# Kernel tuning notes

Hardware: AMD Instinct MI355X
Metric: run time of the kernel (lower is better)

The kernel has to match this reference:

```python
import jax, jax.numpy as jnp
import numpy as np
import math

B, L, V, D, H, DQ, DV, DI, NL, BOARD = 2048, 10, 1974, 512, 8, 64, 64, 2048, 6, 70
SCALE = 0.02

def _ln(x, g, b):
    m = x.mean(-1, keepdims=True)
    v = ((x - m) ** 2).mean(-1, keepdims=True)
    return (x - m) * jax.lax.rsqrt(v + 1e-5) * g + b

def _mha(x, kv, ln_g, ln_b, wq, bq, wkv, bkv, wo, bo, key_mask, causal, self_attn):
    # residual + pre-LN multi-head attention, as in the torch module (dropout in eval mode = identity)
    res = x
    xn = _ln(x, ln_g, ln_b)
    kvn = _ln(kv, ln_g, ln_b) if self_attn else kv  # torch code layer-norms KV only for self-attention
    b, lq, _ = x.shape
    lk = kv.shape[1]
    q = (xn @ wq + bq).reshape(b, lq, H, DQ)
    kvp = kvn @ wkv + bkv
    k = kvp[..., : H * DQ].reshape(b, lk, H, DQ)
    v = kvp[..., H * DQ :].reshape(b, lk, H, DV)
    s = jnp.einsum('bqhd,bkhd->bhqk', q, k) * (1.0 / math.sqrt(DQ))  # (B,H,Lq,Lk)
    if key_mask is not None:
        s = jnp.where(key_mask[:, None, None, :], s, -jnp.inf)
    if causal:
        s = jnp.where(jnp.tril(jnp.ones((lq, lk), bool)), s, -jnp.inf)
    a = jax.nn.softmax(s, axis=-1)
    o = jnp.einsum('bhqk,bkhd->bqhd', a, v).reshape(b, lq, H * DV)
    return o @ wo + bo + res

def _ffn(x, ln_g, ln_b, w1, b1, w2, b2):
    h = jax.nn.relu(_ln(x, ln_g, ln_b) @ w1 + b1)
    return h @ w2 + b2 + x

def _forward(moves, lengths, boards, emb, pos, sa_ln_g, sa_ln_b, sa_wq, sa_bq, sa_wkv, sa_bkv, sa_wo, sa_bo, ca_ln_g, ca_ln_b, ca_wq, ca_bq, ca_wkv, ca_bkv, ca_wo, ca_bo, ff_ln_g, ff_ln_b, ff_w1, ff_b1, ff_w2, ff_b2, fin_g, fin_b, fc_w, fc_b):
    x = emb[moves] * math.sqrt(D) + pos[None, :, :]  # (B,L,D)
    key_mask = jnp.arange(L)[None, :] < lengths[:, None]  # (B,L) valid move positions
    for i in range(NL):
        x = _mha(x, x, sa_ln_g[i], sa_ln_b[i], sa_wq[i], sa_bq[i], sa_wkv[i], sa_bkv[i], sa_wo[i], sa_bo[i], key_mask, True, True)
        x = _mha(x, boards, ca_ln_g[i], ca_ln_b[i], ca_wq[i], ca_bq[i], ca_wkv[i], ca_bkv[i], ca_wo[i], ca_bo[i], None, False, False)
        x = _ffn(x, ff_ln_g[i], ff_ln_b[i], ff_w1[i], ff_b1[i], ff_w2[i], ff_b2[i])
    x = _ln(x, fin_g, fin_b)
    return x @ fc_w + fc_b  # (B,L,V) logits

def setup_inputs():
    key = jax.random.key(0)
    ks = iter(jax.random.split(key, 40))
    n = lambda shape: jax.random.normal(next(ks), shape, dtype=jnp.float32) * SCALE
    return {
        'moves': jax.random.randint(next(ks), (B, L), 0, V),
        'lengths': jax.random.randint(next(ks), (B,), 1, L + 1),
        'boards': jax.random.normal(next(ks), (B, BOARD, D), dtype=jnp.float32),
        'emb': n((V, D)),
        'pos': n((L, D)),
        'sa_ln_g': jnp.ones((NL, D)), 'sa_ln_b': jnp.zeros((NL, D)),
        'sa_wq': n((NL, D, H * DQ)), 'sa_bq': jnp.zeros((NL, H * DQ)),
        'sa_wkv': n((NL, D, H * (DQ + DV))), 'sa_bkv': jnp.zeros((NL, H * (DQ + DV))),
        'sa_wo': n((NL, H * DV, D)), 'sa_bo': jnp.zeros((NL, D)),
        'ca_ln_g': jnp.ones((NL, D)), 'ca_ln_b': jnp.zeros((NL, D)),
        'ca_wq': n((NL, D, H * DQ)), 'ca_bq': jnp.zeros((NL, H * DQ)),
        'ca_wkv': n((NL, D, H * (DQ + DV))), 'ca_bkv': jnp.zeros((NL, H * (DQ + DV))),
        'ca_wo': n((NL, H * DV, D)), 'ca_bo': jnp.zeros((NL, D)),
        'ff_ln_g': jnp.ones((NL, D)), 'ff_ln_b': jnp.zeros((NL, D)),
        'ff_w1': n((NL, D, DI)), 'ff_b1': jnp.zeros((NL, DI)),
        'ff_w2': n((NL, DI, D)), 'ff_b2': jnp.zeros((NL, D)),
        'fin_g': jnp.ones((D,)), 'fin_b': jnp.zeros((D,)),
        'fc_w': n((D, V)), 'fc_b': jnp.zeros((V,)),
    }

def reference(moves, lengths, boards, emb, pos, sa_ln_g, sa_ln_b, sa_wq, sa_bq, sa_wkv, sa_bkv, sa_wo, sa_bo, ca_ln_g, ca_ln_b, ca_wq, ca_bq, ca_wkv, ca_bkv, ca_wo, ca_bo, ff_ln_g, ff_ln_b, ff_w1, ff_b1, ff_w2, ff_b2, fin_g, fin_b, fc_w, fc_b):
    return _forward(moves, lengths, boards, emb, pos, sa_ln_g, sa_ln_b, sa_wq, sa_bq, sa_wkv, sa_bkv, sa_wo, sa_bo, ca_ln_g, ca_ln_b, ca_wq, ca_bq, ca_wkv, ca_bkv, ca_wo, ca_bo, ff_ln_g, ff_ln_b, ff_w1, ff_b1, ff_w2, ff_b2, fin_g, fin_b, fc_w, fc_b)
```

## Files before the change

kernel.cpp:

```cpp
#include <hip/hip_runtime.h>
#include <math.h>

#define B_     2048
#define L_     10
#define D_     512
#define H_     8
#define V_     1974
#define DI_    2048
#define NL_    6
#define BOARD_ 70
#define ROWS_  (B_ * L_)
#define SQRT_D 22.627416997969522f

typedef __attribute__((ext_vector_type(8))) short s16x8;
typedef __attribute__((ext_vector_type(4))) float f32x4;

__device__ __forceinline__ void split2(float x, short &hi, short &lo)
{
    unsigned u = __float_as_uint(x);
    hi = (short)(u >> 16);
    float hf = __uint_as_float(u & 0xffff0000u);
    lo = (short)(__float_as_uint(x - hf) >> 16);
}

__global__ __launch_bounds__(256)
void embed_k(const int* __restrict__ moves, const float* __restrict__ emb,
             const float* __restrict__ pos, float* __restrict__ X)
{
    int idx = blockIdx.x * 256 + threadIdx.x;
    if (idx >= ROWS_ * D_) return;
    int d  = idx & 511;
    int bl = idx >> 9;
    int l  = bl % L_;
    int mv = moves[bl];
    X[idx] = emb[mv * D_ + d] * SQRT_D + pos[l * D_ + d];
}

__global__ __launch_bounds__(256)
void ln_k(const float* __restrict__ X, const float* __restrict__ g,
          const float* __restrict__ bta, float* __restrict__ Y, int rows)
{
    int wave = threadIdx.x >> 6;
    int lane = threadIdx.x & 63;
    int row  = blockIdx.x * 4 + wave;
    if (row >= rows) return;
    const float* x = X + (size_t)row * D_;
    float4 t0 = *(const float4*)&x[lane * 8];
    float4 t1 = *(const float4*)&x[lane * 8 + 4];
    float v[8] = { t0.x, t0.y, t0.z, t0.w, t1.x, t1.y, t1.z, t1.w };
    float s1 = 0.f, s2 = 0.f;
    #pragma unroll
    for (int q = 0; q < 8; q++) { s1 += v[q]; s2 += v[q] * v[q]; }
    #pragma unroll
    for (int off = 32; off; off >>= 1) {
        s1 += __shfl_xor(s1, off);
        s2 += __shfl_xor(s2, off);
    }
    float m   = s1 * (1.f / D_);
    float var = s2 * (1.f / D_) - m * m;
    float r   = 1.0f / sqrtf(var + 1e-5f);
    float* y = Y + (size_t)row * D_;
    #pragma unroll
    for (int q = 0; q < 8; q++) {
        int d = lane * 8 + q;
        y[d] = (v[q] - m) * r * g[d] + bta[d];
    }
}

__global__ __launch_bounds__(256)
void tsplit_k(const float* __restrict__ W, short* __restrict__ Thi,
              short* __restrict__ Tlo, int K, int N)
{
    __shared__ float t[32][33];
    int n0 = blockIdx.x * 32, k0 = blockIdx.y * 32;
    int c = threadIdx.x & 31, r = threadIdx.x >> 5;
    #pragma unroll
    for (int i = 0; i < 4; i++) {
        int kk = k0 + r + i * 8, nn = n0 + c;
        t[r + i * 8][c] = (nn < N) ? W[(size_t)kk * N + nn] : 0.f;
    }
    __syncthreads();
    #pragma unroll
    for (int i = 0; i < 4; i++) {
        int nn = n0 + r + i * 8;
        int kk = k0 + c;
        if (nn < N) {
            short hi, lo; split2(t[c][r + i * 8], hi, lo);
            Thi[(size_t)nn * K + kk] = hi;
            Tlo[(size_t)nn * K + kk] = lo;
        }
    }
}

template<bool BIAS, bool RELU, bool RESID>
__global__ __launch_bounds__(256)
void mgemm_k(const float* __restrict__ A,
             const short* __restrict__ BThi, const short* __restrict__ BTlo,
             const float* __restrict__ bias, const float* __restrict__ resid,
             float* __restrict__ C, int M, int N, int K)
{
    __shared__ short Ah[4][128][8], Al[4][128][8];
    __shared__ short Bh[4][128][8], Bl[4][128][8];

    const int tid = threadIdx.x;
    const int m0 = blockIdx.y * 128, n0 = blockIdx.x * 128;

    const int ar   = tid >> 2;
    const int akg  = tid & 3;
    const int bc   = tid >> 1;
    const int bkg0 = tid & 1;

    const int lane = tid & 63;
    const int wv   = tid >> 6;
    const int wm   = (wv >> 1) * 64, wn = (wv & 1) * 64;
    const int rsel = lane & 15, kg = lane >> 4;

    f32x4 acc[4][4];
    #pragma unroll
    for (int i = 0; i < 4; i++)
        #pragma unroll
        for (int j = 0; j < 4; j++)
            #pragma unroll
            for (int q = 0; q < 4; q++) acc[i][j][q] = 0.f;

    const s16x8 *pAh[4], *pAl[4], *pBh[4], *pBl[4];
    #pragma unroll
    for (int x = 0; x < 4; x++) {
        pAh[x] = (const s16x8*)&Ah[kg][wm + x * 16 + rsel][0];
        pAl[x] = (const s16x8*)&Al[kg][wm + x * 16 + rsel][0];
        pBh[x] = (const s16x8*)&Bh[kg][wn + x * 16 + rsel][0];
        pBl[x] = (const s16x8*)&Bl[kg][wn + x * 16 + rsel][0];
    }

    f32x4 pa[2][2];
    s16x8 pbh[2], pbl[2];

    auto loadA = [&](int k0) {
        #pragma unroll
        for (int p = 0; p < 2; p++) {
            const float* ap = A + (size_t)(m0 + ar + p * 64) * K + k0 + akg * 8;
            pa[p][0] = *(const f32x4*)ap;
            pa[p][1] = *(const f32x4*)(ap + 4);
        }
    };
    auto loadB = [&](int k0) {
        #pragma unroll
        for (int p = 0; p < 2; p++) {
            int col = n0 + bc, kgp = bkg0 + p * 2;
            if (col < N) {
                size_t off = (size_t)col * K + k0 + kgp * 8;
                pbh[p] = *(const s16x8*)(BThi + off);
                pbl[p] = *(const s16x8*)(BTlo + off);
            } else {
                #pragma unroll
                for (int q = 0; q < 8; q++) { pbh[p][q] = 0; pbl[p][q] = 0; }
            }
        }
    };
    auto storeLDS = [&]() {
        #pragma unroll
        for (int p = 0; p < 2; p++) {
            s16x8 h, l;
            #pragma unroll
            for (int q = 0; q < 8; q++) {
                float x = (q < 4) ? pa[p][0][q] : pa[p][1][q - 4];
                short hh, ll; split2(x, hh, ll);
                h[q] = hh; l[q] = ll;
            }
            *(s16x8*)&Ah[akg][ar + p * 64][0] = h;
            *(s16x8*)&Al[akg][ar + p * 64][0] = l;
            *(s16x8*)&Bh[bkg0 + p * 2][bc][0] = pbh[p];
            *(s16x8*)&Bl[bkg0 + p * 2][bc][0] = pbl[p];
        }
    };

    loadA(0); loadB(0);
    const int nk = K >> 5;
    for (int t = 0; t < nk; t++) {
        __syncthreads();
        storeLDS();
        __syncthreads();
        if (t + 1 < nk) { loadA((t + 1) << 5); loadB((t + 1) << 5); }

        s16x8 a_hi[4], b_hi[4], tmp[4];
        #pragma unroll
        for (int x = 0; x < 4; x++) a_hi[x] = *pAh[x];
        #pragma unroll
        for (int x = 0; x < 4; x++) b_hi[x] = *pBh[x];
        #pragma unroll
        for (int mt = 0; mt < 4; mt++)
            #pragma unroll
            for (int nt = 0; nt < 4; nt++)
                acc[mt][nt] = __builtin_amdgcn_mfma_f32_16x16x32_bf16(
                    a_hi[mt], b_hi[nt], acc[mt][nt], 0, 0, 0);
        #pragma unroll
        for (int x = 0; x < 4; x++) tmp[x] = *pBl[x];
        #pragma unroll
        for (int mt = 0; mt < 4; mt++)
            #pragma unroll
            for (int nt = 0; nt < 4; nt++)
                acc[mt][nt] = __builtin_amdgcn_mfma_f32_16x16x32_bf16(
                    a_hi[mt], tmp[nt], acc[mt][nt], 0, 0, 0);
        #pragma unroll
        for (int x = 0; x < 4; x++) tmp[x] = *pAl[x];
        #pragma unroll
        for (int mt = 0; mt < 4; mt++)
            #pragma unroll
            for (int nt = 0; nt < 4; nt++)
                acc[mt][nt] = __builtin_amdgcn_mfma_f32_16x16x32_bf16(
                    tmp[mt], b_hi[nt], acc[mt][nt], 0, 0, 0);
    }

    #pragma unroll
    for (int mt = 0; mt < 4; mt++) {
        #pragma unroll
        for (int q = 0; q < 4; q++) {
            int m = m0 + wm + mt * 16 + kg * 4 + q;
            #pragma unroll
            for (int nt = 0; nt < 4; nt++) {
                int n = n0 + wn + nt * 16 + rsel;
                if (n < N) {
                    float v = acc[mt][nt][q];
                    if (BIAS)  v += bias[n];
                    if (RELU)  v = fmaxf(v, 0.f);
                    if (RESID) v += resid[(size_t)m * N + n];
                    C[(size_t)m * N + n] = v;
                }
            }
        }
    }
}

template<bool BIAS, bool RELU, bool RESID>
__global__ __launch_bounds__(256)
void gemm_k(const float* __restrict__ A, const float* __restrict__ Bw,
            const float* __restrict__ bias, const float* __restrict__ resid,
            float* __restrict__ C, int M, int N, int K)
{
    __shared__ float As[8][128];
    __shared__ float Bs[8][128];
    const int tid = threadIdx.x;
    const int tx = tid & 15, ty = tid >> 4;
    const int m0 = blockIdx.y * 128, n0 = blockIdx.x * 128;
    float acc[8][8] = {};
    const int arow = tid >> 1;
    const int akk  = (tid & 1) * 4;
    const int brow = tid >> 5;
    const int bcol = (tid & 31) * 4;
    const int am   = m0 + arow;

    for (int k0 = 0; k0 < K; k0 += 8) {
        float a4[4];
        if (am < M) {
            const float* ap = A + (size_t)am * K + k0 + akk;
            float4 t = *(const float4*)ap;
            a4[0] = t.x; a4[1] = t.y; a4[2] = t.z; a4[3] = t.w;
        } else { a4[0] = a4[1] = a4[2] = a4[3] = 0.f; }
        #pragma unroll
        for (int q = 0; q < 4; q++) As[akk + q][arow] = a4[q];
        {
            const int nb = n0 + bcol;
            const float* bp = Bw + (size_t)(k0 + brow) * N + nb;
            float b4[4];
            if (nb + 3 < N) {
                float2 u0 = *(const float2*)bp;
                float2 u1 = *(const float2*)(bp + 2);
                b4[0] = u0.x; b4[1] = u0.y; b4[2] = u1.x; b4[3] = u1.y;
            } else {
                #pragma unroll
                for (int q = 0; q < 4; q++) b4[q] = (nb + q < N) ? bp[q] : 0.f;
            }
            #pragma unroll
            for (int q = 0; q < 4; q++) Bs[brow][bcol + q] = b4[q];
        }
        __syncthreads();
        #pragma unroll
        for (int kk = 0; kk < 8; kk++) {
            float4 a0 = *(const float4*)&As[kk][ty * 8];
            float4 a1 = *(const float4*)&As[kk][ty * 8 + 4];
            float4 b0 = *(const float4*)&Bs[kk][tx * 8];
            float4 b1 = *(const float4*)&Bs[kk][tx * 8 + 4];
            float av[8] = {a0.x,a0.y,a0.z,a0.w,a1.x,a1.y,a1.z,a1.w};
            float bv[8] = {b0.x,b0.y,b0.z,b0.w,b1.x,b1.y,b1.z,b1.w};
            #pragma unroll
            for (int i = 0; i < 8; i++)
                #pragma unroll
                for (int j = 0; j < 8; j++)
                    acc[i][j] += av[i] * bv[j];
        }
        __syncthreads();
    }
    #pragma unroll
    for (int i = 0; i < 8; i++) {
        int m = m0 + ty * 8 + i;
        if (m >= M) continue;
        #pragma unroll
        for (int j = 0; j < 8; j++) {
            int n = n0 + tx * 8 + j;
            if (n >= N) continue;
            float v = acc[i][j];
            if (BIAS)  v += bias[n];
            if (RELU)  v = fmaxf(v, 0.f);
            if (RESID) v += resid[(size_t)m * N + n];
            C[(size_t)m * N + n] = v;
        }
    }
}

__global__ __launch_bounds__(256)
void self_attn_k(const float* __restrict__ Qb, const float* __restrict__ KVP,
                 const int* __restrict__ lengths, float* __restrict__ O, int b0)
{
    __shared__ float qs[L_ * D_];
    __shared__ float ks[L_ * D_];
    __shared__ float vs[L_ * D_];
    __shared__ float sc[H_ * L_ * L_];
    int bl  = blockIdx.x;
    int b   = b0 + bl;
    int tid = threadIdx.x;
    int len = lengths[b];

    for (int p = tid; p < L_ * D_; p += 256) {
        int row = p >> 9, col = p & 511;
        qs[p] = Qb[((size_t)(b * L_ + row)) * D_ + col];
        ks[p] = KVP[((size_t)(bl * L_ + row)) * 1024 + col];
        vs[p] = KVP[((size_t)(bl * L_ + row)) * 1024 + 512 + col];
    }
    __syncthreads();

    for (int p = tid; p < H_ * L_ * L_; p += 256) {
        int h = p / (L_ * L_), r = p % (L_ * L_), i = r / L_, j = r % L_;
        float s = -1e30f;
        if (j <= i && j < len) {
            const float* qq = &qs[i * D_ + h * 64];
            const float* kk = &ks[j * D_ + h * 64];
            float d = 0.f;
            #pragma unroll
            for (int d0 = 0; d0 < 64; d0++) d += qq[d0] * kk[d0];
            s = d * 0.125f;
        }
        sc[p] = s;
    }
    __syncthreads();

    if (tid < H_ * L_) {
        int base = tid * L_;
        float mx = -1e30f;
        for (int j = 0; j < L_; j++) mx = fmaxf(mx, sc[base + j]);
        float sum = 0.f;
        for (int j = 0; j < L_; j++) { float e = expf(sc[base + j] - mx); sc[base + j] = e; sum += e; }
        float inv = 1.f / sum;
        for (int j = 0; j < L_; j++) sc[base + j] *= inv;
    }
    __syncthreads();

    for (int p = tid; p < L_ * D_; p += 256) {
        int i = p >> 9, col = p & 511, h = col >> 6;
        float o = 0.f;
        #pragma unroll
        for (int j = 0; j < L_; j++) o += sc[(h * L_ + i) * L_ + j] * vs[j * D_ + col];
        O[((size_t)(b * L_ + i)) * D_ + col] = o;
    }
}

__global__ __launch_bounds__(256)
void cross_attn_k(const float* __restrict__ Qb, const float* __restrict__ KVP,
                  float* __restrict__ O, int b0)
{
    __shared__ float qs[L_ * 64];
    __shared__ float ks[BOARD_ * 64];
    __shared__ float vs[BOARD_ * 64];
    __shared__ float sc[L_ * BOARD_];
    int blk = blockIdx.x;
    int bl  = blk >> 3;
    int h   = blk & 7;
    int b   = b0 + bl;
    int tid = threadIdx.x;

    for (int p = tid; p < L_ * 64; p += 256) {
        int i = p >> 6, d = p & 63;
        qs[p] = Qb[((size_t)(b * L_ + i)) * D_ + h * 64 + d];
    }
    for (int p = tid; p < BOARD_ * 64; p += 256) {
        int j = p >> 6, d = p & 63;
        size_t kr = (size_t)(bl * BOARD_ + j);
        ks[p] = KVP[kr * 1024 + h * 64 + d];
        vs[p] = KVP[kr * 1024 + 512 + h * 64 + d];
    }
    __syncthreads();

    for (int p = tid; p < L_ * BOARD_; p += 256) {
        int i = p / BOARD_, j = p % BOARD_;
        float d = 0.f;
        #pragma unroll
        for (int d0 = 0; d0 < 64; d0++) d += qs[i * 64 + d0] * ks[j * 64 + d0];
        sc[p] = d * 0.125f;
    }
    __syncthreads();

    if (tid < L_) {
        float mx = -1e30f;
        for (int j = 0; j < BOARD_; j++) mx = fmaxf(mx, sc[tid * BOARD_ + j]);
        float sum = 0.f;
        for (int j = 0; j < BOARD_; j++) {
            float e = expf(sc[tid * BOARD_ + j] - mx);
            sc[tid * BOARD_ + j] = e; sum += e;
        }
        float inv = 1.f / sum;
        for (int j = 0; j < BOARD_; j++) sc[tid * BOARD_ + j] *= inv;
    }
    __syncthreads();

    for (int p = tid; p < L_ * 64; p += 256) {
        int i = p >> 6, d = p & 63;
        float o = 0.f;
        for (int j = 0; j < BOARD_; j++) o += sc[i * BOARD_ + j] * vs[j * 64 + d];
        O[((size_t)(b * L_ + i)) * D_ + h * 64 + d] = o;
    }
}

extern "C" void kernel_launch(void* const* d_in, const int* in_sizes, int n_in,
                              void* d_out, int out_size, void* d_ws, size_t ws_size,
                              hipStream_t stream)
{
    (void)in_sizes; (void)n_in; (void)out_size;
    const int*   moves   = (const int*)d_in[0];
    const int*   lengths = (const int*)d_in[1];
    const float* boards  = (const float*)d_in[2];
    const float* emb     = (const float*)d_in[3];
    const float* pos     = (const float*)d_in[4];
    const float* sa_ln_g = (const float*)d_in[5];
    const float* sa_ln_b = (const float*)d_in[6];
    const float* sa_wq   = (const float*)d_in[7];
    const float* sa_bq   = (const float*)d_in[8];
    const float* sa_wkv  = (const float*)d_in[9];
    const float* sa_bkv  = (const float*)d_in[10];
    const float* sa_wo   = (const float*)d_in[11];
    const float* sa_bo   = (const float*)d_in[12];
    const float* ca_ln_g = (const float*)d_in[13];
    const float* ca_ln_b = (const float*)d_in[14];
    const float* ca_wq   = (const float*)d_in[15];
    const float* ca_bq   = (const float*)d_in[16];
    const float* ca_wkv  = (const float*)d_in[17];
    const float* ca_bkv  = (const float*)d_in[18];
    const float* ca_wo   = (const float*)d_in[19];
    const float* ca_bo   = (const float*)d_in[20];
    const float* ff_ln_g = (const float*)d_in[21];
    const float* ff_ln_b = (const float*)d_in[22];
    const float* ff_w1   = (const float*)d_in[23];
    const float* ff_b1   = (const float*)d_in[24];
    const float* ff_w2   = (const float*)d_in[25];
    const float* ff_b2   = (const float*)d_in[26];
    const float* fin_g   = (const float*)d_in[27];
    const float* fin_b   = (const float*)d_in[28];
    const float* fc_w    = (const float*)d_in[29];
    const float* fc_b    = (const float*)d_in[30];

    float* X  = (float*)d_out;
    float* Q  = X + (size_t)ROWS_ * D_;
    float* U  = Q + (size_t)ROWS_ * D_;
    const size_t WSLAB = (size_t)2048 * 512;
    short* WThi = (short*)(U + (size_t)17920 * 1024);
    short* WTlo = WThi + WSLAB;
    short* QThi = (short*)Q;
    short* QTlo = QThi + WSLAB;
    float* XN = (float*)d_ws;
    short* FThi = (short*)(XN + (size_t)ROWS_ * D_);
    short* FTlo = FThi + WSLAB;
    const bool ws_wt = ws_size >= (size_t)ROWS_ * D_ * 4 + 2 * WSLAB * sizeof(short);

    const int lnGrid = ROWS_ / 4;
    #define TGRID(N, K) dim3(((N) + 31) / 32, (K) / 32)

    embed_k<<<(ROWS_ * D_ + 255) / 256, 256, 0, stream>>>(moves, emb, pos, X);

    for (int i = 0; i < NL_; i++) {
        ln_k<<<lnGrid, 256, 0, stream>>>(X, sa_ln_g + i * D_, sa_ln_b + i * D_, XN, ROWS_);
        tsplit_k<<<TGRID(512, 512), 256, 0, stream>>>(sa_wq + (size_t)i * D_ * 512, WThi, WTlo, 512, 512);
        mgemm_k<true, false, false><<<dim3(4, 160), 256, 0, stream>>>(
            XN, WThi, WTlo, sa_bq + i * 512, nullptr, Q, ROWS_, 512, 512);
        tsplit_k<<<TGRID(1024, 512), 256, 0, stream>>>(sa_wkv + (size_t)i * D_ * 1024, WThi, WTlo, 512, 1024);
        for (int c = 0; c < 2; c++) {
            const int RB = 1024, RR = RB * L_;
            mgemm_k<true, false, false><<<dim3(8, RR / 128), 256, 0, stream>>>(
                XN + (size_t)c * RR * D_, WThi, WTlo, sa_bkv + i * 1024, nullptr,
                U, RR, 1024, 512);
            self_attn_k<<<RB, 256, 0, stream>>>(Q, U, lengths, XN, c * RB);
        }
        tsplit_k<<<TGRID(512, 512), 256, 0, stream>>>(sa_wo + (size_t)i * 512 * D_, WThi, WTlo, 512, 512);
        mgemm_k<true, false, true><<<dim3(4, 160), 256, 0, stream>>>(
            XN, WThi, WTlo, sa_bo + i * D_, X, X, ROWS_, 512, 512);

        ln_k<<<lnGrid, 256, 0, stream>>>(X, ca_ln_g + i * D_, ca_ln_b + i * D_, XN, ROWS_);
        tsplit_k<<<TGRID(512, 512), 256, 0, stream>>>(ca_wq + (size_t)i * D_ * 512, WThi, WTlo, 512, 512);
        mgemm_k<true, false, false><<<dim3(4, 160), 256, 0, stream>>>(
            XN, WThi, WTlo, ca_bq + i * 512, nullptr, Q, ROWS_, 512, 512);
        tsplit_k<<<TGRID(1024, 512), 256, 0, stream>>>(ca_wkv + (size_t)i * D_ * 1024, WThi, WTlo, 512, 1024);
        for (int c = 0; c < B_ / 256; c++) {
            const int CHB = 256, KR = CHB * BOARD_;
            mgemm_k<true, false, false><<<dim3(8, KR / 128), 256, 0, stream>>>(
                boards + (size_t)c * KR * D_, WThi, WTlo, ca_bkv + i * 1024, nullptr,
                U, KR, 1024, 512);
            cross_attn_k<<<CHB * H_, 256, 0, stream>>>(Q, U, XN, c * CHB);
        }
        tsplit_k<<<TGRID(512, 512), 256, 0, stream>>>(ca_wo + (size_t)i * 512 * D_, WThi, WTlo, 512, 512);
        mgemm_k<true, false, true><<<dim3(4, 160), 256, 0, stream>>>(
            XN, WThi, WTlo, ca_bo + i * D_, X, X, ROWS_, 512, 512);

        ln_k<<<lnGrid, 256, 0, stream>>>(X, ff_ln_g + i * D_, ff_ln_b + i * D_, XN, ROWS_);
        tsplit_k<<<TGRID(2048, 512), 256, 0, stream>>>(ff_w1 + (size_t)i * D_ * DI_, QThi, QTlo, 512, 2048);
        tsplit_k<<<TGRID(512, 2048), 256, 0, stream>>>(ff_w2 + (size_t)i * DI_ * D_, WThi, WTlo, 2048, 512);
        for (int rc = 0; rc < 4; rc++) {
            const int RC = ROWS_ / 4;
            mgemm_k<true, true, false><<<dim3(16, RC / 128), 256, 0, stream>>>(
                XN + (size_t)rc * RC * D_, QThi, QTlo, ff_b1 + i * DI_, nullptr,
                U, RC, DI_, 512);
            mgemm_k<true, false, true><<<dim3(4, RC / 128), 256, 0, stream>>>(
                U, WThi, WTlo, ff_b2 + i * D_,
                X + (size_t)rc * RC * D_, X + (size_t)rc * RC * D_, RC, 512, DI_);
        }
    }

    ln_k<<<lnGrid, 256, 0, stream>>>(X, fin_g, fin_b, XN, ROWS_);
    if (ws_wt) {
        tsplit_k<<<TGRID(V_, 512), 256, 0, stream>>>(fc_w, FThi, FTlo, 512, V_);
        mgemm_k<true, false, false><<<dim3((V_ + 127) / 128, 160), 256, 0, stream>>>(
            XN, FThi, FTlo, fc_b, nullptr, (float*)d_out, ROWS_, V_, 512);
    } else {
        gemm_k<true, false, false><<<dim3((V_ + 127) / 128, 160), 256, 0, stream>>>(
            XN, fc_w, fc_b, nullptr, (float*)d_out, ROWS_, V_, 512);
    }
}
```

Before: 15.59 ms.

## Rewrite split-bf16 GEMM with 32x32 MFMA, direct-to-LDS B loads, double buffering

Replaces the split-bf16 MFMA GEMM with a new kernel that uses 32x32x16 MFMA tiles, loads the pre-split weight operand straight into LDS with global_load_lds, and double-buffers the B tile so the next K-step load overlaps compute. It also XOR-swizzles the A tile in LDS to avoid bank conflicts, puts M on the x grid axis, and allows wider N tiles (256) with two blocks per CU. The bounds check in tsplit is removed and the FC split is padded to 2048 columns, so the workspace must hold the padded FC weights. The unguarded B loads rely on the padded N. In exchange the kernel has more register pressure and depends on the workspace padding being correct.

```diff
diff --git a/kernel.cpp b/kernel.cpp
--- a/kernel.cpp
+++ b/kernel.cpp
@@ -12,8 +12,9 @@
 #define ROWS_  (B_ * L_)
 #define SQRT_D 22.627416997969522f
 
-typedef __attribute__((ext_vector_type(8))) short s16x8;
-typedef __attribute__((ext_vector_type(4))) float f32x4;
+typedef __attribute__((ext_vector_type(8)))  short s16x8;
+typedef __attribute__((ext_vector_type(4)))  float f32x4;
+typedef __attribute__((ext_vector_type(16))) float f32x16;
 
 __device__ __forceinline__ void split2(float x, short &hi, short &lo)
 {
@@ -22,6 +23,15 @@
     float hf = __uint_as_float(u & 0xffff0000u);
     lo = (short)(__float_as_uint(x - hf) >> 16);
 }
+
+__device__ __forceinline__ void gload_lds16(const void* g, void* l)
+{
+    __builtin_amdgcn_global_load_lds(
+        (const __attribute__((address_space(1))) unsigned int*)g,
+        (__attribute__((address_space(3))) unsigned int*)l, 16, 0, 0);
+}
+
+__device__ __forceinline__ int gofs(int kg) { return ((kg & 1) << 2) | (kg & 2); }
 
 __global__ __launch_bounds__(256)
 void embed_k(const int* __restrict__ moves, const float* __restrict__ emb,
@@ -84,57 +94,43 @@
     for (int i = 0; i < 4; i++) {
         int nn = n0 + r + i * 8;
         int kk = k0 + c;
-        if (nn < N) {
-            short hi, lo; split2(t[c][r + i * 8], hi, lo);
-            Thi[(size_t)nn * K + kk] = hi;
-            Tlo[(size_t)nn * K + kk] = lo;
-        }
-    }
-}
-
-template<bool BIAS, bool RELU, bool RESID>
-__global__ __launch_bounds__(256)
-void mgemm_k(const float* __restrict__ A,
-             const short* __restrict__ BThi, const short* __restrict__ BTlo,
-             const float* __restrict__ bias, const float* __restrict__ resid,
-             float* __restrict__ C, int M, int N, int K)
-{
+        short hi, lo; split2(t[c][r + i * 8], hi, lo);
+        Thi[(size_t)nn * K + kk] = hi;
+        Tlo[(size_t)nn * K + kk] = lo;
+    }
+}
+
+template<int BN, bool BIAS, bool RELU, bool RESID>
+__global__ __launch_bounds__(256, 2)
+void mg2_k(const float* __restrict__ A,
+           const short* __restrict__ BThi, const short* __restrict__ BTlo,
+           const float* __restrict__ bias, const float* __restrict__ resid,
+           float* __restrict__ C, int M, int N, int K)
+{
+    constexpr int NF = BN / 64;
     __shared__ short Ah[4][128][8], Al[4][128][8];
-    __shared__ short Bh[4][128][8], Bl[4][128][8];
-
-    const int tid = threadIdx.x;
-    const int m0 = blockIdx.y * 128, n0 = blockIdx.x * 128;
-
-    const int ar   = tid >> 2;
-    const int akg  = tid & 3;
-    const int bc   = tid >> 1;
-    const int bkg0 = tid & 1;
-
+    __shared__ short Bh[2][4][BN][8], Bl[2][4][BN][8];
+
+    const int tid  = threadIdx.x;
     const int lane = tid & 63;
     const int wv   = tid >> 6;
-    const int wm   = (wv >> 1) * 64, wn = (wv & 1) * 64;
-    const int rsel = lane & 15, kg = lane >> 4;
-
-    f32x4 acc[4][4];
-    #pragma unroll
-    for (int i = 0; i < 4; i++)
-        #pragma unroll
-        for (int j = 0; j < 4; j++)
-            #pragma unroll
-            for (int q = 0; q < 4; q++) acc[i][j][q] = 0.f;
-
-    const s16x8 *pAh[4], *pAl[4], *pBh[4], *pBl[4];
-    #pragma unroll
-    for (int x = 0; x < 4; x++) {
-        pAh[x] = (const s16x8*)&Ah[kg][wm + x * 16 + rsel][0];
-        pAl[x] = (const s16x8*)&Al[kg][wm + x * 16 + rsel][0];
-        pBh[x] = (const s16x8*)&Bh[kg][wn + x * 16 + rsel][0];
-        pBl[x] = (const s16x8*)&Bl[kg][wn + x * 16 + rsel][0];
-    }
+    const int m0 = blockIdx.x * 128, n0 = blockIdx.y * BN;
+
+    const int ar  = tid >> 2;
+    const int akg = tid & 3;
+
+    const int wm  = (wv >> 1) * 64, wn = (wv & 1) * (BN / 2);
+    const int l31 = lane & 31, lhi = lane >> 5;
+
+    f32x16 acc[2][NF];
+    #pragma unroll
+    for (int mf = 0; mf < 2; mf++)
+        #pragma unroll
+        for (int nf = 0; nf < NF; nf++)
+            #pragma unroll
+            for (int r = 0; r < 16; r++) acc[mf][nf][r] = 0.f;
 
     f32x4 pa[2][2];
-    s16x8 pbh[2], pbl[2];
-
     auto loadA = [&](int k0) {
         #pragma unroll
         for (int p = 0; p < 2; p++) {
@@ -143,21 +139,8 @@
             pa[p][1] = *(const f32x4*)(ap + 4);
         }
     };
-    auto loadB = [&](int k0) {
-        #pragma unroll
-        for (int p = 0; p < 2; p++) {
-            int col = n0 + bc, kgp = bkg0 + p * 2;
-            if (col < N) {
-                size_t off = (size_t)col * K + k0 + kgp * 8;
-                pbh[p] = *(const s16x8*)(BThi + off);
-                pbl[p] = *(const s16x8*)(BTlo + off);
-            } else {
-                #pragma unroll
-                for (int q = 0; q < 8; q++) { pbh[p][q] = 0; pbl[p][q] = 0; }
-            }
-        }
-    };
-    auto storeLDS = [&]() {
+    auto storeA = [&]() {
+        const int g = gofs(akg);
         #pragma unroll
         for (int p = 0; p < 2; p++) {
             s16x8 h, l;
@@ -167,61 +150,84 @@
                 short hh, ll; split2(x, hh, ll);
                 h[q] = hh; l[q] = ll;
             }
-            *(s16x8*)&Ah[akg][ar + p * 64][0] = h;
-            *(s16x8*)&Al[akg][ar + p * 64][0] = l;
-            *(s16x8*)&Bh[bkg0 + p * 2][bc][0] = pbh[p];
-            *(s16x8*)&Bl[bkg0 + p * 2][bc][0] = pbl[p];
+            const int row = (ar + p * 64) ^ g;
+            *(s16x8*)&Ah[akg][row][0] = h;
+            *(s16x8*)&Al[akg][row][0] = l;
         }
     };
-
-    loadA(0); loadB(0);
+    auto issueB = [&](int k0, int bb) {
+        #pragma unroll
+        for (int cb = 0; cb < NF; cb++) {
+            const size_t go = (size_t)(n0 + cb * 64 + lane) * K + k0 + wv * 8;
+            gload_lds16(BThi + go, &Bh[bb][wv][cb * 64][0]);
+            gload_lds16(BTlo + go, &Bl[bb][wv][cb * 64][0]);
+        }
+    };
+    auto compute = [&](int bb) {
+        #pragma unroll
+        for (int ks = 0; ks < 2; ks++) {
+            const int kg = 2 * ks + lhi;
+            const int g  = gofs(kg);
+            s16x8 ah[2], bh[NF], bl[NF], al[2];
+            #pragma unroll
+            for (int mf = 0; mf < 2; mf++)
+                ah[mf] = *(const s16x8*)&Ah[kg][(wm + mf * 32 + l31) ^ g][0];
+            #pragma unroll
+            for (int nf = 0; nf < NF; nf++)
+                bh[nf] = *(const s16x8*)&Bh[bb][kg][wn + nf * 32 + l31][0];
+            #pragma unroll
+            for (int mf = 0; mf < 2; mf++)
+                #pragma unroll
+                for (int nf = 0; nf < NF; nf++)
+                    acc[mf][nf] = __builtin_amdgcn_mfma_f32_32x32x16_bf16(
+                        ah[mf], bh[nf], acc[mf][nf], 0, 0, 0);
+            #pragma unroll
+            for (int nf = 0; nf < NF; nf++)
+                bl[nf] = *(const s16x8*)&Bl[bb][kg][wn + nf * 32 + l31][0];
+            #pragma unroll
+            for (int mf = 0; mf < 2; mf++)
+                #pragma unroll
+                for (int nf = 0; nf < NF; nf++)
+                    acc[mf][nf] = __builtin_amdgcn_mfma_f32_32x32x16_bf16(
+                        ah[mf], bl[nf], acc[mf][nf], 0, 0, 0);
+            #pragma unroll
+            for (int mf = 0; mf < 2; mf++)
+                al[mf] = *(const s16x8*)&Al[kg][(wm + mf * 32 + l31) ^ g][0];
+            #pragma unroll
+            for (int mf = 0; mf < 2; mf++)
+                #pragma unroll
+                for (int nf = 0; nf < NF; nf++)
+                    acc[mf][nf] = __builtin_amdgcn_mfma_f32_32x32x16_bf16(
+                        al[mf], bh[nf], acc[mf][nf], 0, 0, 0);
+        }
+    };
+
+    issueB(0, 0);
+    loadA(0);
+    __syncthreads();
     const int nk = K >> 5;
     for (int t = 0; t < nk; t++) {
+        storeA();
         __syncthreads();
-        storeLDS();
+        if (t + 1 < nk) {
+            issueB((t + 1) << 5, (t + 1) & 1);
+            loadA((t + 1) << 5);
+        }
+        compute(t & 1);
         __syncthreads();
-        if (t + 1 < nk) { loadA((t + 1) << 5); loadB((t + 1) << 5); }
-
-        s16x8 a_hi[4], b_hi[4], tmp[4];
-        #pragma unroll
-        for (int x = 0; x < 4; x++) a_hi[x] = *pAh[x];
-        #pragma unroll
-        for (int x = 0; x < 4; x++) b_hi[x] = *pBh[x];
-        #pragma unroll
-        for (int mt = 0; mt < 4; mt++)
-            #pragma unroll
-            for (int nt = 0; nt < 4; nt++)
-                acc[mt][nt] = __builtin_amdgcn_mfma_f32_16x16x32_bf16(
-                    a_hi[mt], b_hi[nt], acc[mt][nt], 0, 0, 0);
-        #pragma unroll
-        for (int x = 0; x < 4; x++) tmp[x] = *pBl[x];
-        #pragma unroll
-        for (int mt = 0; mt < 4; mt++)
-            #pragma unroll
-            for (int nt = 0; nt < 4; nt++)
-                acc[mt][nt] = __builtin_amdgcn_mfma_f32_16x16x32_bf16(
-                    a_hi[mt], tmp[nt], acc[mt][nt], 0, 0, 0);
-        #pragma unroll
-        for (int x = 0; x < 4; x++) tmp[x] = *pAl[x];
-        #pragma unroll
-        for (int mt = 0; mt < 4; mt++)
-            #pragma unroll
-            for (int nt = 0; nt < 4; nt++)
-                acc[mt][nt] = __builtin_amdgcn_mfma_f32_16x16x32_bf16(
-                    tmp[mt], b_hi[nt], acc[mt][nt], 0, 0, 0);
-    }
-
-    #pragma unroll
-    for (int mt = 0; mt < 4; mt++) {
-        #pragma unroll
-        for (int q = 0; q < 4; q++) {
-            int m = m0 + wm + mt * 16 + kg * 4 + q;
-            #pragma unroll
-            for (int nt = 0; nt < 4; nt++) {
-                int n = n0 + wn + nt * 16 + rsel;
-                if (n < N) {
-                    float v = acc[mt][nt][q];
-                    if (BIAS)  v += bias[n];
+    }
+
+    #pragma unroll
+    for (int mf = 0; mf < 2; mf++) {
+        #pragma unroll
+        for (int nf = 0; nf < NF; nf++) {
+            const int n = n0 + wn + nf * 32 + l31;
+            if (n < N) {
+                const float bv = BIAS ? bias[n] : 0.f;
+                #pragma unroll
+                for (int r = 0; r < 16; r++) {
+                    const int m = m0 + wm + mf * 32 + (r & 3) + 8 * (r >> 2) + 4 * lhi;
+                    float v = acc[mf][nf][r] + bv;
                     if (RELU)  v = fmaxf(v, 0.f);
                     if (RESID) v += resid[(size_t)m * N + n];
                     C[(size_t)m * N + n] = v;
@@ -477,34 +483,34 @@
     for (int i = 0; i < NL_; i++) {
         ln_k<<<lnGrid, 256, 0, stream>>>(X, sa_ln_g + i * D_, sa_ln_b + i * D_, XN, ROWS_);
         tsplit_k<<<TGRID(512, 512), 256, 0, stream>>>(sa_wq + (size_t)i * D_ * 512, WThi, WTlo, 512, 512);
-        mgemm_k<true, false, false><<<dim3(4, 160), 256, 0, stream>>>(
+        mg2_k<128, true, false, false><<<dim3(160, 4), 256, 0, stream>>>(
             XN, WThi, WTlo, sa_bq + i * 512, nullptr, Q, ROWS_, 512, 512);
         tsplit_k<<<TGRID(1024, 512), 256, 0, stream>>>(sa_wkv + (size_t)i * D_ * 1024, WThi, WTlo, 512, 1024);
         for (int c = 0; c < 2; c++) {
             const int RB = 1024, RR = RB * L_;
-            mgemm_k<true, false, false><<<dim3(8, RR / 128), 256, 0, stream>>>(
+            mg2_k<256, true, false, false><<<dim3(RR / 128, 4), 256, 0, stream>>>(
                 XN + (size_t)c * RR * D_, WThi, WTlo, sa_bkv + i * 1024, nullptr,
                 U, RR, 1024, 512);
             self_attn_k<<<RB, 256, 0, stream>>>(Q, U, lengths, XN, c * RB);
         }
         tsplit_k<<<TGRID(512, 512), 256, 0, stream>>>(sa_wo + (size_t)i * 512 * D_, WThi, WTlo, 512, 512);
-        mgemm_k<true, false, true><<<dim3(4, 160), 256, 0, stream>>>(
+        mg2_k<128, true, false, true><<<dim3(160, 4), 256, 0, stream>>>(
             XN, WThi, WTlo, sa_bo + i * D_, X, X, ROWS_, 512, 512);
 
         ln_k<<<lnGrid, 256, 0, stream>>>(X, ca_ln_g + i * D_, ca_ln_b + i * D_, XN, ROWS_);
         tsplit_k<<<TGRID(512, 512), 256, 0, stream>>>(ca_wq + (size_t)i * D_ * 512, WThi, WTlo, 512, 512);
-        mgemm_k<true, false, false><<<dim3(4, 160), 256, 0, stream>>>(
+        mg2_k<128, true, false, false><<<dim3(160, 4), 256, 0, stream>>>(
             XN, WThi, WTlo, ca_bq + i * 512, nullptr, Q, ROWS_, 512, 512);
         tsplit_k<<<TGRID(1024, 512), 256, 0, stream>>>(ca_wkv + (size_t)i * D_ * 1024, WThi, WTlo, 512, 1024);
         for (int c = 0; c < B_ / 256; c++) {
             const int CHB = 256, KR = CHB * BOARD_;
-            mgemm_k<true, false, false><<<dim3(8, KR / 128), 256, 0, stream>>>(
+            mg2_k<256, true, false, false><<<dim3(KR / 128, 4), 256, 0, stream>>>(
                 boards + (size_t)c * KR * D_, WThi, WTlo, ca_bkv + i * 1024, nullptr,
                 U, KR, 1024, 512);
             cross_attn_k<<<CHB * H_, 256, 0, stream>>>(Q, U, XN, c * CHB);
         }
         tsplit_k<<<TGRID(512, 512), 256, 0, stream>>>(ca_wo + (size_t)i * 512 * D_, WThi, WTlo, 512, 512);
-        mgemm_k<true, false, true><<<dim3(4, 160), 256, 0, stream>>>(
+        mg2_k<128, true, false, true><<<dim3(160, 4), 256, 0, stream>>>(
             XN, WThi, WTlo, ca_bo + i * D_, X, X, ROWS_, 512, 512);
 
         ln_k<<<lnGrid, 256, 0, stream>>>(X, ff_ln_g + i * D_, ff_ln_b + i * D_, XN, ROWS_);
@@ -512,10 +518,10 @@
         tsplit_k<<<TGRID(512, 2048), 256, 0, stream>>>(ff_w2 + (size_t)i * DI_ * D_, WThi, WTlo, 2048, 512);
         for (int rc = 0; rc < 4; rc++) {
             const int RC = ROWS_ / 4;
-            mgemm_k<true, true, false><<<dim3(16, RC / 128), 256, 0, stream>>>(
+            mg2_k<256, true, true, false><<<dim3(RC / 128, 8), 256, 0, stream>>>(
                 XN + (size_t)rc * RC * D_, QThi, QTlo, ff_b1 + i * DI_, nullptr,
                 U, RC, DI_, 512);
-            mgemm_k<true, false, true><<<dim3(4, RC / 128), 256, 0, stream>>>(
+            mg2_k<128, true, false, true><<<dim3(RC / 128, 4), 256, 0, stream>>>(
                 U, WThi, WTlo, ff_b2 + i * D_,
                 X + (size_t)rc * RC * D_, X + (size_t)rc * RC * D_, RC, 512, DI_);
         }
@@ -523,8 +529,8 @@
 
     ln_k<<<lnGrid, 256, 0, stream>>>(X, fin_g, fin_b, XN, ROWS_);
     if (ws_wt) {
-        tsplit_k<<<TGRID(V_, 512), 256, 0, stream>>>(fc_w, FThi, FTlo, 512, V_);
-        mgemm_k<true, false, false><<<dim3((V_ + 127) / 128, 160), 256, 0, stream>>>(
+        tsplit_k<<<dim3(2048 / 32, 512 / 32), 256, 0, stream>>>(fc_w, FThi, FTlo, 512, V_);
+        mg2_k<256, true, false, false><<<dim3(160, 8), 256, 0, stream>>>(
             XN, FThi, FTlo, fc_b, nullptr, (float*)d_out, ROWS_, V_, 512);
     } else {
         gemm_k<true, false, false><<<dim3((V_ + 127) / 128, 160), 256, 0, stream>>>(
```

New measurement: 14.44 ms. -7.4%, faster.
